# Kernel tuning notes

Measured on AMD Instinct MI355X. Metric: run time of the kernel, lower is better.

Reference implementation:

```python
import jax, jax.numpy as jnp
import numpy as np
from jax import lax

G, K, KS = 4, 16, 3            # stripes, latents per stripe, support kernel
TEMP, TOPK_RATIO, GATE, EPS = 0.125, 0.125, 0.05, 1e-6


def _l2norm(v):
    # F.normalize(p=2, dim=-1): divide by max(norm, 1e-12)
    return v / jnp.maximum(jnp.linalg.norm(v, axis=-1, keepdims=True), 1e-12)


def _avg_pool3(x):
    # 3x3 avg pool, stride 1, pad 1, count_include_pad=True (torch default)
    s = lax.reduce_window(x, 0.0, lax.add, (1, 1, KS, KS), (1, 1, 1, 1),
                          [(0, 0), (0, 0), (KS // 2, KS // 2), (KS // 2, KS // 2)])
    return s / float(KS * KS)


def setup_inputs() -> dict:
    key = jax.random.key(0)
    k1, k2 = jax.random.split(key)
    x = jax.random.normal(k1, (64, 256, 64, 44), dtype=jnp.float32)
    latent_basis = jax.random.normal(k2, (G, K, 256), dtype=jnp.float32) * 0.05
    return {"x": x, "latent_basis": latent_basis}


def reference(x, latent_basis):
    n, c, h, w = x.shape
    hs = h // G
    # 'n c (g hs) w -> (n g) c hs w'
    sf = x.reshape(n, c, G, hs, w).transpose(0, 2, 1, 3, 4).reshape(n * G, c, hs, w)
    support_feat = _avg_pool3(sf)
    feat_flat = sf.reshape(n, G, c, hs * w).transpose(0, 1, 3, 2)          # n g p c
    supp_flat = support_feat.reshape(n, G, c, hs * w).transpose(0, 1, 3, 2)  # n g p c
    # active mask from detached energy
    e = jnp.mean(lax.stop_gradient(sf) ** 2, axis=1)                       # [n*G, hs, w]
    e = e / jnp.maximum(jnp.max(e, axis=(-2, -1), keepdims=True), EPS)
    am = (e > GATE).astype(jnp.float32)
    fb = (e > 0).astype(jnp.float32)
    use_fb = jnp.sum(am, axis=(-2, -1), keepdims=True) <= 0
    am = jnp.where(use_fb, fb, am).reshape(n, G, hs * w)                   # n g p
    # routing
    sfn = _l2norm(supp_flat)
    lb = _l2norm(latent_basis)                                             # g k c
    logits = jnp.einsum('ngpc,gkc->ngpk', sfn, lb) / TEMP
    route = jax.nn.softmax(logits, axis=-1)
    supp = route * am[..., None]                                           # n g p k
    pw = supp / jnp.maximum(jnp.sum(supp, axis=2, keepdims=True), EPS)
    tokens = jnp.einsum('ngpk,ngpc->ngkc', pw, feat_flat)                  # n g k c
    tokens = tokens.transpose(0, 3, 1, 2).reshape(n, c, G * K)             # n c (g k)
    # presence via top-k over positions
    p = supp.shape[2]
    topk = max(1, min(p, int(p * TOPK_RATIO)))
    vals = lax.top_k(supp.transpose(0, 1, 3, 2), topk)[0]                  # n g k topk
    pres = jnp.mean(vals, axis=-1).reshape(n, G * K)
    pres = pres / jnp.maximum(jnp.sum(pres, axis=1, keepdims=True), EPS)
    return tokens, pres
```

## Files before the change

### kernel.cpp

```cpp
#include <hip/hip_runtime.h>
#include <cstdint>


#define C_ 256
#define W_ 44
#define P_ 704
#define CH_STRIDE 2816
#define NB_STRIDE 720896
#define TOPK_ 88
#define GATE_ 0.05f
#define EPS_ 1e-6f

__global__ __launch_bounds__(256) void k_norm_basis(const float* __restrict__ lb,
                                                    float* __restrict__ lbn) {
  int gk = blockIdx.x;
  int t = threadIdx.x;
  float v = lb[gk * 256 + t];
  float ss = v * v;
  #pragma unroll
  for (int off = 32; off >= 1; off >>= 1) ss += __shfl_xor(ss, off);
  __shared__ float red[4];
  if ((t & 63) == 0) red[t >> 6] = ss;
  __syncthreads();
  float tot = red[0] + red[1] + red[2] + red[3];
  float scale = 1.f / fmaxf(sqrtf(tot), 1e-12f);
  int g = gk >> 4, k = gk & 15;
  lbn[((g * 256 + t) << 4) + k] = v * scale;
}

__global__ __launch_bounds__(1024) void k_route(const float* __restrict__ x,
                                                const float* __restrict__ lbn,
                                                float* __restrict__ supp_kp,
                                                float* __restrict__ supp_pk,
                                                float* __restrict__ invden_ws) {
  __shared__ float lbn_l[4096];
  __shared__ float rsl[11264];
  __shared__ float redA[16];
  __shared__ float redB[16];
  __shared__ float redM[2];
  __shared__ float red2[16 * 16];

  const int tid = threadIdx.x;
  const int w = tid >> 6;
  const int l = tid & 63;
  const bool act = (l < 44);
  const int s = blockIdx.x, n = s >> 2, g = s & 3;
  const int p = w * 44 + l;

  for (int i = tid; i < 4096; i += 1024) lbn_l[i] = lbn[(g << 12) + i];

  const int lsafe = act ? l : 0;
  const float* xb = x + (size_t)n * NB_STRIDE + (g * 16 + w) * 44 + lsafe;
  const float* xm = xb + ((w > 0)  ? -44 : 0);
  const float* xp = xb + ((w < 15) ?  44 : 0);
  const bool hm = (w > 0), hp = (w < 15);

  float rawdot[16];
  #pragma unroll
  for (int k = 0; k < 16; k++) rawdot[k] = 0.f;
  float sq = 0.f, pw2 = 0.f;

  __syncthreads();

  for (int c = 0; c < 256; c += 4) {
    float vm[4], v0[4], vp[4];
    #pragma unroll
    for (int j = 0; j < 4; j++) {
      const size_t o = (size_t)(c + j) * CH_STRIDE;
      vm[j] = xm[o]; v0[j] = xb[o]; vp[j] = xp[o];
    }
    #pragma unroll
    for (int j = 0; j < 4; j++) {
      float a  = act ? v0[j] : 0.f;
      float am_ = (act && hm) ? vm[j] : 0.f;
      float ap_ = (act && hp) ? vp[j] : 0.f;
      float vs = am_ + a + ap_;
      float lf = __shfl(vs, (l + 63) & 63);
      float rt = __shfl(vs, (l + 1) & 63);
      float win = lf + vs + rt;
      pw2 = fmaf(win, win, pw2);
      sq  = fmaf(a, a, sq);
      const float4* wp = (const float4*)&lbn_l[(c + j) << 4];
      float4 w0 = wp[0], w1 = wp[1], w2 = wp[2], w3 = wp[3];
      rawdot[0]  = fmaf(a, w0.x, rawdot[0]);  rawdot[1]  = fmaf(a, w0.y, rawdot[1]);
      rawdot[2]  = fmaf(a, w0.z, rawdot[2]);  rawdot[3]  = fmaf(a, w0.w, rawdot[3]);
      rawdot[4]  = fmaf(a, w1.x, rawdot[4]);  rawdot[5]  = fmaf(a, w1.y, rawdot[5]);
      rawdot[6]  = fmaf(a, w1.z, rawdot[6]);  rawdot[7]  = fmaf(a, w1.w, rawdot[7]);
      rawdot[8]  = fmaf(a, w2.x, rawdot[8]);  rawdot[9]  = fmaf(a, w2.y, rawdot[9]);
      rawdot[10] = fmaf(a, w2.z, rawdot[10]); rawdot[11] = fmaf(a, w2.w, rawdot[11]);
      rawdot[12] = fmaf(a, w3.x, rawdot[12]); rawdot[13] = fmaf(a, w3.y, rawdot[13]);
      rawdot[14] = fmaf(a, w3.z, rawdot[14]); rawdot[15] = fmaf(a, w3.w, rawdot[15]);
    }
  }

  float e_raw = sq * (1.f / 256.f);
  float m = e_raw;
  #pragma unroll
  for (int off = 32; off >= 1; off >>= 1) m = fmaxf(m, __shfl_xor(m, off));
  if (l == 0) redA[w] = m;
  __syncthreads();
  if (tid == 0) {
    float mm = redA[0];
    for (int w2 = 1; w2 < 16; w2++) mm = fmaxf(mm, redA[w2]);
    redM[0] = mm;
  }
  __syncthreads();
  float M = fmaxf(redM[0], EPS_);
  float e = e_raw / M;
  float am = (e > GATE_) ? 1.f : 0.f;
  float fb = (e_raw > 0.f) ? 1.f : 0.f;
  float a = am;
  #pragma unroll
  for (int off = 32; off >= 1; off >>= 1) a += __shfl_xor(a, off);
  if (l == 0) redB[w] = a;
  __syncthreads();
  if (tid == 0) {
    float sm = 0.f;
    for (int w2 = 0; w2 < 16; w2++) sm += redB[w2];
    redM[1] = sm;
  }
  __syncthreads();
  if (redM[1] <= 0.f) am = fb;

  if (act) {
    #pragma unroll
    for (int k = 0; k < 16; k++) rsl[k * 704 + p] = rawdot[k];
  }
  __syncthreads();

  float pd[16];
  #pragma unroll
  for (int k = 0; k < 16; k++) pd[k] = 0.f;
  if (act) {
    #pragma unroll
    for (int dy = -1; dy <= 1; dy++) {
      int yy = w + dy;
      if (yy < 0 || yy > 15) continue;
      #pragma unroll
      for (int dx = -1; dx <= 1; dx++) {
        int xx = l + dx;
        if (xx < 0 || xx > 43) continue;
        int pp = yy * 44 + xx;
        #pragma unroll
        for (int k = 0; k < 16; k++) pd[k] += rsl[k * 704 + pp];
      }
    }
  }

  float pnorm = sqrtf(pw2) * (1.f / 9.f);
  float invn = 1.f / fmaxf(pnorm, 1e-12f);
  float scl = invn * (8.f / 9.f);
  float li[16];
  float mx = -1e30f;
  #pragma unroll
  for (int k = 0; k < 16; k++) { li[k] = pd[k] * scl; mx = fmaxf(mx, li[k]); }
  float ssum = 0.f;
  #pragma unroll
  for (int k = 0; k < 16; k++) { li[k] = __expf(li[k] - mx); ssum += li[k]; }
  float rs2 = am / ssum;
  float supp[16];
  #pragma unroll
  for (int k = 0; k < 16; k++) supp[k] = li[k] * rs2;

  if (act) {
    float* sbp = supp_kp + (size_t)s * (16 * 704);
    #pragma unroll
    for (int k = 0; k < 16; k++) sbp[k * 704 + p] = supp[k];
    float* spk = supp_pk + ((size_t)s * 704 + p) * 16;
    #pragma unroll
    for (int kq = 0; kq < 4; kq++)
      ((float4*)spk)[kq] = make_float4(supp[kq*4+0], supp[kq*4+1],
                                       supp[kq*4+2], supp[kq*4+3]);
  }

  #pragma unroll
  for (int k = 0; k < 16; k++) {
    float v2 = act ? supp[k] : 0.f;
    #pragma unroll
    for (int off = 32; off >= 1; off >>= 1) v2 += __shfl_xor(v2, off);
    if (l == 0) red2[w * 16 + k] = v2;
  }
  __syncthreads();
  if (tid < 16) {
    float den = 0.f;
    for (int w2 = 0; w2 < 16; w2++) den += red2[w2 * 16 + tid];
    invden_ws[s * 16 + tid] = 1.f / fmaxf(den, EPS_);
  }
}

__global__ __launch_bounds__(256) void k_topk(const float* __restrict__ supp_kp,
                                              float* __restrict__ presraw) {
  const int blk = blockIdx.x;
  const int t = threadIdx.x;
  const int lane = t & 63, w = t >> 6;
  const float* v = supp_kp + (size_t)blk * 704;
  const bool h2 = (t < 192);
  uint32_t key0 = __float_as_uint(v[t]);
  uint32_t key1 = __float_as_uint(v[t + 256]);
  uint32_t key2 = h2 ? __float_as_uint(v[t + 512]) : 0u;

  __shared__ uint32_t hist[256];
  __shared__ uint32_t sarr[257];
  __shared__ uint32_t wsum[4];
  __shared__ uint32_t bc0, bc1;
  uint32_t prefix = 0, remaining = TOPK_;

  for (int b = 3; b >= 0; b--) {
    hist[t] = 0u;
    __syncthreads();
    const int shift = b * 8;
    uint32_t mhi = (b == 3) ? 0u : (0xFFFFFFFFu << (shift + 8));
    if ((key0 & mhi) == (prefix & mhi)) atomicAdd(&hist[(key0 >> shift) & 255u], 1u);
    if ((key1 & mhi) == (prefix & mhi)) atomicAdd(&hist[(key1 >> shift) & 255u], 1u);
    if (h2 && ((key2 & mhi) == (prefix & mhi))) atomicAdd(&hist[(key2 >> shift) & 255u], 1u);
    __syncthreads();

    uint32_t val = hist[t];
    #pragma unroll
    for (int off = 1; off < 64; off <<= 1) {
      uint32_t o = (uint32_t)__shfl_down((int)val, off);
      if (lane + off < 64) val += o;
    }
    if (lane == 0) wsum[w] = val;
    __syncthreads();
    uint32_t add = 0;
    for (int w2 = w + 1; w2 < 4; w2++) add += wsum[w2];
    sarr[t] = val + add;
    if (t == 0) sarr[256] = 0u;
    __syncthreads();
    uint32_t s_t = sarr[t], s_n = sarr[t + 1];
    if (s_t >= remaining && s_n < remaining) {
      bc0 = prefix | ((uint32_t)t << shift);
      bc1 = remaining - s_n;
    }
    __syncthreads();
    prefix = bc0; remaining = bc1;
    __syncthreads();
  }

  float tf = __uint_as_float(prefix);
  float sgt = 0.f;
  uint32_t cgt = 0;
  if (key0 > prefix) { sgt += __uint_as_float(key0); cgt++; }
  if (key1 > prefix) { sgt += __uint_as_float(key1); cgt++; }
  if (h2 && key2 > prefix) { sgt += __uint_as_float(key2); cgt++; }
  #pragma unroll
  for (int off = 32; off >= 1; off >>= 1) {
    sgt += __shfl_xor(sgt, off);
    cgt += __shfl_xor(cgt, off);
  }
  __shared__ float rsx[4];
  __shared__ uint32_t rcx[4];
  if (lane == 0) { rsx[w] = sgt; rcx[w] = cgt; }
  __syncthreads();
  if (t == 0) {
    float stot = rsx[0] + rsx[1] + rsx[2] + rsx[3];
    uint32_t ctot = rcx[0] + rcx[1] + rcx[2] + rcx[3];
    float top = stot + (float)(TOPK_ - ctot) * tf;
    presraw[blk] = top * (1.f / (float)TOPK_);
  }
}

__global__ __launch_bounds__(512, 4) void k_tokens(const float* __restrict__ x,
                                                   const float* __restrict__ supp_pk,
                                                   const float* __restrict__ invden,
                                                   float* __restrict__ out) {
  __shared__ float xl[4096];
  const int tid = threadIdx.x;
  const int bid = blockIdx.x;
  const int s = bid >> 1, chalf = bid & 1;
  const int n = s >> 2, g = s & 3;
  const int cl = tid & 127;
  const int q = tid >> 7;
  const int sblk = s * (704 * 16);

  const float* xs = x + (size_t)n * NB_STRIDE + (size_t)(chalf * 128) * CH_STRIDE + g * P_;

  const int li0 = tid, li1 = tid + 512;
  const int lc0 = li0 >> 3, lj0 = li0 & 7;
  const int lc1 = li1 >> 3, lj1 = li1 & 7;
  const float* gp0 = xs + (size_t)lc0 * CH_STRIDE + lj0 * 4;
  const float* gp1 = xs + (size_t)lc1 * CH_STRIDE + lj1 * 4;
  const int wo0 = lc0 * 32 + ((lj0 * 4) ^ ((lc0 & 7) * 4));
  const int wo1 = lc1 * 32 + ((lj1 * 4) ^ ((lc1 & 7) * 4));

  const int sw = (cl & 7) * 4;
  const int rbase = cl * 32;

  float acc[16];
  #pragma unroll
  for (int k = 0; k < 16; k++) acc[k] = 0.f;

  float4 r0 = *(const float4*)gp0;
  float4 r1 = *(const float4*)gp1;
  *(float4*)&xl[wo0] = r0;
  *(float4*)&xl[wo1] = r1;
  __syncthreads();

  for (int tt = 0; tt < 22; tt++) {
    const int p0 = tt * 32;
    float4 n0, n1;
    if (tt < 21) {
      n0 = *(const float4*)(gp0 + p0 + 32);
      n1 = *(const float4*)(gp1 + p0 + 32);
    }

    #pragma unroll
    for (int jj = 0; jj < 8; jj += 4) {
      const int pp0 = q * 8 + jj;
      float4 xv = *(const float4*)&xl[rbase + (pp0 ^ sw)];
      float xa[4] = {xv.x, xv.y, xv.z, xv.w};
      #pragma unroll
      for (int dj = 0; dj < 4; dj++) {
        int uofs = __builtin_amdgcn_readfirstlane(sblk + (p0 + pp0 + dj) * 16);
        const float4* sp = (const float4*)(supp_pk + uofs);
        float4 s0 = sp[0], s1 = sp[1], s2 = sp[2], s3 = sp[3];
        float a = xa[dj];
        acc[0]  += a * s0.x; acc[1]  += a * s0.y; acc[2]  += a * s0.z; acc[3]  += a * s0.w;
        acc[4]  += a * s1.x; acc[5]  += a * s1.y; acc[6]  += a * s1.z; acc[7]  += a * s1.w;
        acc[8]  += a * s2.x; acc[9]  += a * s2.y; acc[10] += a * s2.z; acc[11] += a * s2.w;
        acc[12] += a * s3.x; acc[13] += a * s3.y; acc[14] += a * s3.z; acc[15] += a * s3.w;
      }
    }

    __syncthreads();
    if (tt < 21) {
      *(float4*)&xl[wo0] = n0;
      *(float4*)&xl[wo1] = n1;
      __syncthreads();
    }
  }

  if (q >= 2) {
    float* dst = &xl[((q - 2) * 128 + cl) * 16];
    #pragma unroll
    for (int kq = 0; kq < 4; kq++)
      ((float4*)dst)[kq] = make_float4(acc[kq*4], acc[kq*4+1], acc[kq*4+2], acc[kq*4+3]);
  }
  __syncthreads();
  if (q < 2) {
    const float* src = &xl[(q * 128 + cl) * 16];
    #pragma unroll
    for (int k = 0; k < 16; k++) acc[k] += src[k];
  }
  __syncthreads();
  if (q == 1) {
    float* dst = &xl[cl * 16];
    #pragma unroll
    for (int kq = 0; kq < 4; kq++)
      ((float4*)dst)[kq] = make_float4(acc[kq*4], acc[kq*4+1], acc[kq*4+2], acc[kq*4+3]);
  }
  __syncthreads();
  if (q == 0) {
    const float* src = &xl[cl * 16];
    float* op = out + ((size_t)(n * 256 + chalf * 128 + cl) * 64) + g * 16;
    #pragma unroll
    for (int kq = 0; kq < 4; kq++) {
      int u = __builtin_amdgcn_readfirstlane(s * 16 + kq * 4);
      const float4 iv = *(const float4*)(invden + u);
      float4 o;
      o.x = (acc[kq*4+0] + src[kq*4+0]) * iv.x;
      o.y = (acc[kq*4+1] + src[kq*4+1]) * iv.y;
      o.z = (acc[kq*4+2] + src[kq*4+2]) * iv.z;
      o.w = (acc[kq*4+3] + src[kq*4+3]) * iv.w;
      ((float4*)op)[kq] = o;
    }
  }
}

__global__ __launch_bounds__(64) void k_pres(const float* __restrict__ presraw,
                                             float* __restrict__ out) {
  const int n = blockIdx.x, t = threadIdx.x;
  float v = presraw[n * 64 + t];
  float ssum = v;
  #pragma unroll
  for (int off = 32; off >= 1; off >>= 1) ssum += __shfl_xor(ssum, off);
  out[1048576 + n * 64 + t] = v / fmaxf(ssum, EPS_);
}

extern "C" void kernel_launch(void* const* d_in, const int* in_sizes, int n_in,
                              void* d_out, int out_size, void* d_ws, size_t ws_size,
                              hipStream_t stream) {
  (void)in_sizes; (void)n_in; (void)out_size; (void)ws_size;
  const float* x  = (const float*)d_in[0];
  const float* lb = (const float*)d_in[1];
  float* out = (float*)d_out;
  float* ws = (float*)d_ws;
  float* lbn_ws     = ws;
  float* invden_ws  = ws + 16384;
  float* presraw_ws = ws + 20480;
  float* supp_kp_ws = ws + 24576;
  float* supp_pk_ws = ws + 2908160;

  k_norm_basis<<<64, 256, 0, stream>>>(lb, lbn_ws);
  k_route<<<256, 1024, 0, stream>>>(x, lbn_ws, supp_kp_ws, supp_pk_ws, invden_ws);
  k_topk<<<4096, 256, 0, stream>>>(supp_kp_ws, presraw_ws);
  k_tokens<<<512, 512, 0, stream>>>(x, supp_pk_ws, invden_ws, out);
  k_pres<<<64, 64, 0, stream>>>(presraw_ws, out);
}
```

Before: 357.8 us.

## Split routing kernel over channel halves with separate finalize kernel

The routing kernel is split into a dot-product kernel and a finalize kernel. The dot-product kernel runs 512 blocks, each covering half of the channels, and writes partial pooled logits plus squared-sum statistics to workspace. The finalize kernel adds the two halves, then does the energy gating, softmax and writes. This doubles the block count to fill more compute units, at the cost of an extra launch and extra global traffic for the partial results. The partials reuse the supp buffers and the output buffer as scratch. The launch bound of 8 blocks of 1024 threads may also squeeze registers.

```diff
diff --git a/kernel.cpp b/kernel.cpp
--- a/kernel.cpp
+++ b/kernel.cpp
@@ -28,29 +28,28 @@
   lbn[((g * 256 + t) << 4) + k] = v * scale;
 }
 
-__global__ __launch_bounds__(1024) void k_route(const float* __restrict__ x,
-                                                const float* __restrict__ lbn,
-                                                float* __restrict__ supp_kp,
-                                                float* __restrict__ supp_pk,
-                                                float* __restrict__ invden_ws) {
-  __shared__ float lbn_l[4096];
+__global__ __launch_bounds__(1024, 8) void k_route_dot(const float* __restrict__ x,
+                                                       const float* __restrict__ lbn,
+                                                       float* __restrict__ pd0,
+                                                       float* __restrict__ pd1,
+                                                       float* __restrict__ sqpw) {
+  __shared__ float lbn_l[2048];
   __shared__ float rsl[11264];
-  __shared__ float redA[16];
-  __shared__ float redB[16];
-  __shared__ float redM[2];
-  __shared__ float red2[16 * 16];
 
   const int tid = threadIdx.x;
   const int w = tid >> 6;
   const int l = tid & 63;
   const bool act = (l < 44);
-  const int s = blockIdx.x, n = s >> 2, g = s & 3;
+  const int bid = blockIdx.x;
+  const int s = bid >> 1, half = bid & 1;
+  const int n = s >> 2, g = s & 3;
   const int p = w * 44 + l;
 
-  for (int i = tid; i < 4096; i += 1024) lbn_l[i] = lbn[(g << 12) + i];
+  for (int i = tid; i < 2048; i += 1024) lbn_l[i] = lbn[(g << 12) + (half << 11) + i];
 
   const int lsafe = act ? l : 0;
-  const float* xb = x + (size_t)n * NB_STRIDE + (g * 16 + w) * 44 + lsafe;
+  const float* xb = x + (size_t)n * NB_STRIDE + (size_t)(half * 128) * CH_STRIDE
+                      + (g * 16 + w) * 44 + lsafe;
   const float* xm = xb + ((w > 0)  ? -44 : 0);
   const float* xp = xb + ((w < 15) ?  44 : 0);
   const bool hm = (w > 0), hp = (w < 15);
@@ -62,7 +61,7 @@
 
   __syncthreads();
 
-  for (int c = 0; c < 256; c += 4) {
+  for (int c = 0; c < 128; c += 4) {
     float vm[4], v0[4], vp[4];
     #pragma unroll
     for (int j = 0; j < 4; j++) {
@@ -93,35 +92,6 @@
     }
   }
 
-  float e_raw = sq * (1.f / 256.f);
-  float m = e_raw;
-  #pragma unroll
-  for (int off = 32; off >= 1; off >>= 1) m = fmaxf(m, __shfl_xor(m, off));
-  if (l == 0) redA[w] = m;
-  __syncthreads();
-  if (tid == 0) {
-    float mm = redA[0];
-    for (int w2 = 1; w2 < 16; w2++) mm = fmaxf(mm, redA[w2]);
-    redM[0] = mm;
-  }
-  __syncthreads();
-  float M = fmaxf(redM[0], EPS_);
-  float e = e_raw / M;
-  float am = (e > GATE_) ? 1.f : 0.f;
-  float fb = (e_raw > 0.f) ? 1.f : 0.f;
-  float a = am;
-  #pragma unroll
-  for (int off = 32; off >= 1; off >>= 1) a += __shfl_xor(a, off);
-  if (l == 0) redB[w] = a;
-  __syncthreads();
-  if (tid == 0) {
-    float sm = 0.f;
-    for (int w2 = 0; w2 < 16; w2++) sm += redB[w2];
-    redM[1] = sm;
-  }
-  __syncthreads();
-  if (redM[1] <= 0.f) am = fb;
-
   if (act) {
     #pragma unroll
     for (int k = 0; k < 16; k++) rsl[k * 704 + p] = rawdot[k];
@@ -146,6 +116,78 @@
       }
     }
   }
+
+  if (act) {
+    float* dst = (half ? pd1 : pd0) + (size_t)s * 11264 + p * 16;
+    #pragma unroll
+    for (int kq = 0; kq < 4; kq++)
+      ((float4*)dst)[kq] = make_float4(pd[kq*4+0], pd[kq*4+1], pd[kq*4+2], pd[kq*4+3]);
+    *(float2*)(sqpw + ((size_t)(s * 2 + half) * 704 + p) * 2) = make_float2(sq, pw2);
+  }
+}
+
+__global__ __launch_bounds__(1024) void k_route_fin(float* __restrict__ supp_kp,
+                                                    float* __restrict__ supp_pk,
+                                                    const float* __restrict__ sqpw,
+                                                    float* __restrict__ invden_ws) {
+  __shared__ float redA[16];
+  __shared__ float redB[16];
+  __shared__ float redM[2];
+  __shared__ float red2[16 * 16];
+
+  const int tid = threadIdx.x;
+  const int w = tid >> 6;
+  const int l = tid & 63;
+  const bool act = (l < 44);
+  const int s = blockIdx.x;
+  const int p = w * 44 + l;
+
+  float pd[16];
+  #pragma unroll
+  for (int k = 0; k < 16; k++) pd[k] = 0.f;
+  float sq = 0.f, pw2 = 0.f;
+  if (act) {
+    const float4* a0 = (const float4*)(supp_kp + (size_t)s * 11264 + p * 16);
+    const float4* a1 = (const float4*)(supp_pk + (size_t)s * 11264 + p * 16);
+    #pragma unroll
+    for (int kq = 0; kq < 4; kq++) {
+      float4 u = a0[kq], v = a1[kq];
+      pd[kq*4+0] = u.x + v.x; pd[kq*4+1] = u.y + v.y;
+      pd[kq*4+2] = u.z + v.z; pd[kq*4+3] = u.w + v.w;
+    }
+    float2 s0 = *(const float2*)(sqpw + ((size_t)(s * 2 + 0) * 704 + p) * 2);
+    float2 s1 = *(const float2*)(sqpw + ((size_t)(s * 2 + 1) * 704 + p) * 2);
+    sq = s0.x + s1.x; pw2 = s0.y + s1.y;
+  }
+
+  float e_raw = sq * (1.f / 256.f);
+  float m = e_raw;
+  #pragma unroll
+  for (int off = 32; off >= 1; off >>= 1) m = fmaxf(m, __shfl_xor(m, off));
+  if (l == 0) redA[w] = m;
+  __syncthreads();
+  if (tid == 0) {
+    float mm = redA[0];
+    for (int w2 = 1; w2 < 16; w2++) mm = fmaxf(mm, redA[w2]);
+    redM[0] = mm;
+  }
+  __syncthreads();
+  float M = fmaxf(redM[0], EPS_);
+  float e = e_raw / M;
+  float am = (e > GATE_) ? 1.f : 0.f;
+  float fb = (e_raw > 0.f) ? 1.f : 0.f;
+  float a = am;
+  #pragma unroll
+  for (int off = 32; off >= 1; off >>= 1) a += __shfl_xor(a, off);
+  if (l == 0) redB[w] = a;
+  __syncthreads();
+  if (tid == 0) {
+    float sm = 0.f;
+    for (int w2 = 0; w2 < 16; w2++) sm += redB[w2];
+    redM[1] = sm;
+  }
+  __syncthreads();
+  if (redM[1] <= 0.f) am = fb;
 
   float pnorm = sqrtf(pw2) * (1.f / 9.f);
   float invn = 1.f / fmaxf(pnorm, 1e-12f);
@@ -391,9 +433,11 @@
   float* presraw_ws = ws + 20480;
   float* supp_kp_ws = ws + 24576;
   float* supp_pk_ws = ws + 2908160;
+  float* sqpw_ws    = out;
 
   k_norm_basis<<<64, 256, 0, stream>>>(lb, lbn_ws);
-  k_route<<<256, 1024, 0, stream>>>(x, lbn_ws, supp_kp_ws, supp_pk_ws, invden_ws);
+  k_route_dot<<<512, 1024, 0, stream>>>(x, lbn_ws, supp_kp_ws, supp_pk_ws, sqpw_ws);
+  k_route_fin<<<256, 1024, 0, stream>>>(supp_kp_ws, supp_pk_ws, sqpw_ws, invden_ws);
   k_topk<<<4096, 256, 0, stream>>>(supp_kp_ws, presraw_ws);
   k_tokens<<<512, 512, 0, stream>>>(x, supp_pk_ws, invden_ws, out);
   k_pres<<<64, 64, 0, stream>>>(presraw_ws, out);
```

Result: no change. 360.3 us (+0.7%).
